# Kernel tuning notes

Hardware: AMD Instinct MI355X
Metric: run time of the kernel (lower is better)

The kernel has to match this reference:

```python
import jax, jax.numpy as jnp
import numpy as np


def _maxpool2(x):
    # x: [B, C, H, W] -> 2x2 max pool, stride 2
    b, c, h, w = x.shape
    return x.reshape(b, c, h // 2, 2, w // 2, 2).max(axis=(3, 5))


def _conv1x1(x, w, b):
    # x: [B, Cin, H, W], w: [Cout, Cin], b: [Cout]
    return jnp.einsum('bchw,oc->bohw', x, w) + b[None, :, None, None]


def setup_inputs() -> dict:
    key = jax.random.key(0)
    ks = jax.random.split(key, 8)
    C = 64
    B, H, W = 2, 128, 128
    s = 1.0 / np.sqrt(C)
    return {
        'x': jax.random.normal(ks[0], (B, C, H, W), jnp.float32),
        'w_theta': jax.random.normal(ks[1], (C // 8, C), jnp.float32) * s,
        'b_theta': jax.random.normal(ks[2], (C // 8,), jnp.float32) * s,
        'w_phi': jax.random.normal(ks[3], (C // 8, C), jnp.float32) * s,
        'b_phi': jax.random.normal(ks[4], (C // 8,), jnp.float32) * s,
        'w_g': jax.random.normal(ks[5], (C, C), jnp.float32) * s,
        'b_g': jax.random.normal(ks[6], (C,), jnp.float32) * s,
        'sigma_ratio': jnp.zeros((1,), jnp.float32) + 0.5,
    }


def reference(x, w_theta, b_theta, w_phi, b_phi, w_g, b_g, sigma_ratio):
    b, c, h, w = x.shape
    n = h * w
    # queries: [B, N, C//8]
    theta = _conv1x1(x, w_theta, b_theta).reshape(b, c // 8, n).transpose(0, 2, 1)
    # pooled keys: [B, C//8, N//4]
    phi = _maxpool2(_conv1x1(x, w_phi, b_phi)).reshape(b, c // 8, n // 4)
    # attention: [B, N, N//4] (unscaled, as in original)
    attn = jax.nn.softmax(jnp.einsum('bnd,bdm->bnm', theta, phi), axis=-1)
    # pooled values: [B, N//4, C]
    g = _maxpool2(_conv1x1(x, w_g, b_g)).reshape(b, c, n // 4).transpose(0, 2, 1)
    attn_g = jnp.einsum('bnm,bmc->bnc', attn, g)  # [B, N, C]
    attn_g = attn_g.transpose(0, 2, 1).reshape(b, c, h, w)
    return x + sigma_ratio * attn_g
```

## Files before the change

### kernel.cpp

```cpp
#include <hip/hip_runtime.h>
#include <hip/hip_bf16.h>

typedef _Float16 half8 __attribute__((ext_vector_type(8)));
typedef _Float16 f16x8 __attribute__((ext_vector_type(8)));
typedef __fp16 fp16x2 __attribute__((ext_vector_type(2)));
typedef __bf16 bf16x2v __attribute__((ext_vector_type(2)));
typedef __bf16 bf16x8 __attribute__((ext_vector_type(8)));
typedef float f32x16 __attribute__((ext_vector_type(16)));
typedef unsigned uint2v __attribute__((ext_vector_type(2)));

#define NPIX 16384
#define NPOOL 4096
#define BN 32768
#define KSPLIT 4
#define CHUNK 1024
#define NSTEP 8
#define LOG2E 1.44269504088896340736f

__device__ inline f32x16 mfma16(half8 a, half8 b, f32x16 c) {
  return __builtin_amdgcn_mfma_f32_32x32x16_f16(a, b, c, 0, 0, 0);
}
__device__ inline f32x16 mfma16b(bf16x8 a, bf16x8 b, f32x16 c) {
  return __builtin_amdgcn_mfma_f32_32x32x16_bf16(a, b, c, 0, 0, 0);
}
__device__ inline float fast_exp2(float x) {
#if __has_builtin(__builtin_amdgcn_exp2f)
  return __builtin_amdgcn_exp2f(x);
#else
  return exp2f(x);
#endif
}

__global__ __launch_bounds__(256) void prep_kernel(
    const float* __restrict__ x,
    const float* __restrict__ w_theta, const float* __restrict__ b_theta,
    const float* __restrict__ w_phi, const float* __restrict__ b_phi,
    const float* __restrict__ w_g, const float* __restrict__ b_g,
    _Float16* __restrict__ qf, _Float16* __restrict__ phiT,
    __bf16* __restrict__ gT) {
  __shared__ float xs[64][256];
  int bid = blockIdx.x;
  int oh = bid & 1;
  int pr = (bid >> 1) & 63;
  int b  = bid >> 7;
  int t = threadIdx.x;

  const float* xb = x + (size_t)b * 64 * NPIX + pr * 256;
#pragma unroll 8
  for (int c = 0; c < 64; c++) xs[c][t] = xb[(size_t)c * NPIX + t];
  __syncthreads();

  if (oh == 0) {
    float acc[8];
#pragma unroll
    for (int j = 0; j < 8; j++) acc[j] = b_theta[j];
#pragma unroll 4
    for (int c = 0; c < 64; c++) {
      float xv = xs[c][t];
#pragma unroll
      for (int j = 0; j < 8; j++) acc[j] += xv * w_theta[j * 64 + c];
    }
    half8 h;
#pragma unroll
    for (int j = 0; j < 8; j++) h[j] = (_Float16)(acc[j] * LOG2E);
    *(half8*)(qf + ((size_t)b * NPIX + pr * 256 + t) * 8) = h;
  }

  int pos = t & 63;
  int ocg = t >> 6;
  int oc0 = oh * 36 + ocg * 9;
  const float* wrow[9];
  float a0[9], a1[9], a2[9], a3[9];
#pragma unroll
  for (int j = 0; j < 9; j++) {
    int oc = oc0 + j;
    float bv;
    if (oc < 64) { wrow[j] = w_g + oc * 64; bv = b_g[oc]; }
    else         { wrow[j] = w_phi + (oc - 64) * 64; bv = b_phi[oc - 64]; }
    a0[j] = bv; a1[j] = bv; a2[j] = bv; a3[j] = bv;
  }
#pragma unroll 4
  for (int c = 0; c < 64; c++) {
    float2 lo = *(const float2*)&xs[c][2 * pos];
    float2 hi = *(const float2*)&xs[c][128 + 2 * pos];
#pragma unroll
    for (int j = 0; j < 9; j++) {
      float wv = wrow[j][c];
      a0[j] += wv * lo.x;
      a1[j] += wv * lo.y;
      a2[j] += wv * hi.x;
      a3[j] += wv * hi.y;
    }
  }
  int m = pr * 64 + pos;
#pragma unroll
  for (int j = 0; j < 9; j++) {
    int oc = oc0 + j;
    float v = fmaxf(fmaxf(a0[j], a1[j]), fmaxf(a2[j], a3[j]));
    if (oc < 64) gT[((size_t)b * 64 + oc) * NPOOL + m] = (__bf16)v;
    else         phiT[((size_t)b * NPOOL + m) * 8 + (oc - 64)] = (_Float16)v;
  }
}

__global__ __launch_bounds__(256, 4) void attn_kernel(
    const _Float16* __restrict__ qf, const _Float16* __restrict__ phiT,
    const __bf16* __restrict__ gT,
    float* __restrict__ part_l, _Float16* __restrict__ part_o) {
  __shared__ __bf16 lds_g[2][128 * 64];
  int bx = blockIdx.x;
  int kc = bx & (KSPLIT - 1);
  int qt = (bx >> 2) & 127;
  int b  = bx >> 9;
  int tid = threadIdx.x;
  int lane = tid & 63;
  int w = tid >> 6;
  int q = lane & 31, hi = lane >> 5;
  int qg0 = qt * 128 + w * 32;
  size_t qrow = (size_t)b * NPIX + qg0 + q;

  half8 qfrag = {0, 0, 0, 0, 0, 0, 0, 0};
  if (!hi) qfrag = *(const half8*)(qf + qrow * 8);

  f32x16 oacc0, oacc1;
#pragma unroll
  for (int i = 0; i < 16; i++) { oacc0[i] = 0.f; oacc1[i] = 0.f; }
  float lsum = 0.f;

  int kb0 = kc * CHUNK;

  const __bf16* gbase0;
  const __bf16* gbase1;
  {
    int c0 = (w * 2 + 0) * 8 + (lane >> 3);
    int c1 = (w * 2 + 1) * 8 + (lane >> 3);
    int s  = (lane & 7) ^ (lane >> 3);
    gbase0 = gT + ((size_t)b * 64 + c0) * NPOOL + 8 * s;
    gbase1 = gT + ((size_t)b * 64 + c1) * NPOOL + 8 * s;
  }
#define STAGE(buf, kb)                                                        \
  do {                                                                        \
    __builtin_amdgcn_global_load_lds(                                         \
        (const __attribute__((address_space(1))) void*)(gbase0 + (kb)),       \
        (__attribute__((address_space(3))) void*)((char*)&lds_g[buf][0] +     \
                                                  (w * 2 + 0) * 1024),        \
        16, 0, 0);                                                            \
    __builtin_amdgcn_global_load_lds(                                         \
        (const __attribute__((address_space(1))) void*)(gbase1 + (kb)),       \
        (__attribute__((address_space(3))) void*)((char*)&lds_g[buf][0] +     \
                                                  (w * 2 + 1) * 1024),        \
        16, 0, 0);                                                            \
    __builtin_amdgcn_global_load_lds(                                         \
        (const __attribute__((address_space(1))) void*)(gbase0 + (kb) + 64),  \
        (__attribute__((address_space(3))) void*)((char*)&lds_g[buf][0] +     \
                                                  8192 + (w * 2 + 0) * 1024), \
        16, 0, 0);                                                            \
    __builtin_amdgcn_global_load_lds(                                         \
        (const __attribute__((address_space(1))) void*)(gbase1 + (kb) + 64),  \
        (__attribute__((address_space(3))) void*)((char*)&lds_g[buf][0] +     \
                                                  8192 + (w * 2 + 1) * 1024), \
        16, 0, 0);                                                            \
  } while (0)

  STAGE(0, kb0);
  __syncthreads();
  int cur = 0;

#pragma unroll 1
  for (int step = 0; step < NSTEP; ++step) {
    int kb = kb0 + step * 128;
    if (step + 1 < NSTEP) STAGE(cur ^ 1, kb + 128);
#pragma unroll
    for (int kk = 0; kk < 2; ++kk) {
      int kbb = kb + kk * 64;
      half8 aphi0 = {0, 0, 0, 0, 0, 0, 0, 0}, aphi1 = aphi0;
      if (!hi) {
        aphi0 = *(const half8*)(phiT + ((size_t)b * NPOOL + kbb + q) * 8);
        aphi1 = *(const half8*)(phiT + ((size_t)b * NPOOL + kbb + 32 + q) * 8);
      }
      const __bf16* ldsb = &lds_g[cur][kk * 4096];
#pragma unroll
      for (int sub = 0; sub < 2; ++sub) {
        half8 aphi = sub ? aphi1 : aphi0;
        f32x16 sacc;
#pragma unroll
        for (int i = 0; i < 16; i++) sacc[i] = 0.f;
        sacc = mfma16(aphi, qfrag, sacc);
        float p[16];
#pragma unroll
        for (int i = 0; i < 16; i++) p[i] = fast_exp2(sacc[i]);
        lsum += (((p[0] + p[1]) + (p[2] + p[3])) + ((p[4] + p[5]) + (p[6] + p[7]))) +
                (((p[8] + p[9]) + (p[10] + p[11])) + ((p[12] + p[13]) + (p[14] + p[15])));
#pragma unroll
        for (int halfk = 0; halfk < 2; ++halfk) {
          int pb = halfk * 8;
          bf16x2v t0 = {(__bf16)p[pb + 0], (__bf16)p[pb + 1]};
          bf16x2v t1 = {(__bf16)p[pb + 2], (__bf16)p[pb + 3]};
          bf16x2v t2 = {(__bf16)p[pb + 4], (__bf16)p[pb + 5]};
          bf16x2v t3 = {(__bf16)p[pb + 6], (__bf16)p[pb + 7]};
          unsigned A0 = __builtin_bit_cast(unsigned, t0);
          unsigned A1 = __builtin_bit_cast(unsigned, t1);
          unsigned B0 = __builtin_bit_cast(unsigned, t2);
          unsigned B1 = __builtin_bit_cast(unsigned, t3);
          union { unsigned u[4]; bf16x8 h; } pf;
#if __has_builtin(__builtin_amdgcn_permlane32_swap)
          uint2v r0 = __builtin_amdgcn_permlane32_swap(A0, B0, false, false);
          uint2v r1 = __builtin_amdgcn_permlane32_swap(A1, B1, false, false);
          pf.u[0] = r0[0]; pf.u[1] = r1[0]; pf.u[2] = r0[1]; pf.u[3] = r1[1];
#else
          unsigned xA0 = __shfl_xor(A0, 32), xA1 = __shfl_xor(A1, 32);
          unsigned xB0 = __shfl_xor(B0, 32), xB1 = __shfl_xor(B1, 32);
          pf.u[0] = hi ? xB0 : A0;
          pf.u[1] = hi ? xB1 : A1;
          pf.u[2] = hi ? B0 : xA0;
          pf.u[3] = hi ? B1 : xA1;
#endif
          int sread = sub * 4 + halfk * 2 + hi;
          __builtin_amdgcn_s_setprio(1);
#pragma unroll
          for (int ct = 0; ct < 2; ++ct) {
            int row = ct * 32 + q;
            bf16x8 ag = *(const bf16x8*)(ldsb + row * 64 +
                                         (((16 * sread) ^ ((row & 7) << 4)) >> 1));
            if (ct == 0) oacc0 = mfma16b(ag, pf.h, oacc0);
            else         oacc1 = mfma16b(ag, pf.h, oacc1);
          }
          __builtin_amdgcn_s_setprio(0);
        }
      }
    }
    if (step + 1 < NSTEP) { __syncthreads(); cur ^= 1; }
  }
  lsum += __shfl_xor(lsum, 32);
  float rl = 1.0f / lsum;
  if (!hi) part_l[(size_t)kc * BN + qrow] = lsum;
  _Float16* po = part_o + (((size_t)(kc * 2 + b) * NPIX) + qg0 + q) * 64;
#pragma unroll
  for (int ct = 0; ct < 2; ++ct) {
#pragma unroll
    for (int g = 0; g < 4; ++g) {
      float v0 = (ct ? oacc1[4 * g + 0] : oacc0[4 * g + 0]) * rl;
      float v1 = (ct ? oacc1[4 * g + 1] : oacc0[4 * g + 1]) * rl;
      float v2 = (ct ? oacc1[4 * g + 2] : oacc0[4 * g + 2]) * rl;
      float v3 = (ct ? oacc1[4 * g + 3] : oacc0[4 * g + 3]) * rl;
      uint2v u;
      u[0] = __builtin_bit_cast(unsigned, __builtin_amdgcn_cvt_pkrtz(v0, v1));
      u[1] = __builtin_bit_cast(unsigned, __builtin_amdgcn_cvt_pkrtz(v2, v3));
      *(uint2v*)(po + 32 * ct + 8 * g + 4 * hi) = u;
    }
  }
}

__global__ __launch_bounds__(256) void reduce_kernel(
    const float* __restrict__ part_l, const _Float16* __restrict__ part_o,
    const float* __restrict__ x, const float* __restrict__ sig,
    float* __restrict__ out) {
  int t = threadIdx.x;
  int cg = t >> 6;
  int qi = blockIdx.x * 64 + (t & 63);
  int b = qi >> 14, n = qi & (NPIX - 1);
  float lv[KSPLIT], L = 0.f;
#pragma unroll
  for (int kc = 0; kc < KSPLIT; kc++) {
    lv[kc] = part_l[(size_t)kc * BN + qi];
    L += lv[kc];
  }
  float o16[16];
#pragma unroll
  for (int j = 0; j < 16; j++) o16[j] = 0.f;
#pragma unroll
  for (int kc = 0; kc < KSPLIT; kc++) {
    const _Float16* po = part_o + (((size_t)(kc * 2 + b) * NPIX) + n) * 64 + cg * 16;
    f16x8 v0 = *(const f16x8*)po;
    f16x8 v1 = *(const f16x8*)(po + 8);
    float wv = lv[kc];
#pragma unroll
    for (int j = 0; j < 8; j++) {
      o16[j]     += wv * (float)v0[j];
      o16[8 + j] += wv * (float)v1[j];
    }
  }
  float scale = sig[0] / L;
#pragma unroll
  for (int j = 0; j < 16; j++) {
    int c = cg * 16 + j;
    size_t idx = ((size_t)b * 64 + c) * NPIX + n;
    out[idx] = x[idx] + scale * o16[j];
  }
}

extern "C" void kernel_launch(void* const* d_in, const int* in_sizes, int n_in,
                              void* d_out, int out_size, void* d_ws, size_t ws_size,
                              hipStream_t stream) {
  const float* x       = (const float*)d_in[0];
  const float* w_theta = (const float*)d_in[1];
  const float* b_theta = (const float*)d_in[2];
  const float* w_phi   = (const float*)d_in[3];
  const float* b_phi   = (const float*)d_in[4];
  const float* w_g     = (const float*)d_in[5];
  const float* b_g     = (const float*)d_in[6];
  const float* sigma   = (const float*)d_in[7];
  float* out = (float*)d_out;

  char* ws = (char*)d_ws;
  _Float16* qf     = (_Float16*)ws;
  _Float16* phiT   = (_Float16*)(ws + 524288);
  __bf16*   gT     = (__bf16*)(ws + 655360);
  float*    part_l = (float*)(ws + 1703936);
  _Float16* part_o = (_Float16*)(ws + 2228224);

  prep_kernel<<<256, 256, 0, stream>>>(x, w_theta, b_theta, w_phi, b_phi,
                                       w_g, b_g, qf, phiT, gT);
  attn_kernel<<<2 * 128 * KSPLIT, 256, 0, stream>>>(qf, phiT, gT,
                                                    part_l, part_o);
  reduce_kernel<<<512, 256, 0, stream>>>(part_l, part_o, x, sigma, out);
}
```

Before: 63.80 us.

## Process two query tiles per wave and double the key split

Each wave now handles 64 queries as two 32-row fragments that share every LDS load of the pooled values and phi fragment. This halves LDS traffic per MFMA and gives more independent MFMA chains to interleave. The key dimension is split eight ways instead of four so the grid keeps the same block count. In exchange, accumulator registers roughly double (occupancy bound lowered to 3 blocks), and the larger partial-output buffer adds traffic to the reduce kernel.

```diff
diff --git a/kernel.cpp b/kernel.cpp
--- a/kernel.cpp
+++ b/kernel.cpp
@@ -3,7 +3,6 @@
 
 typedef _Float16 half8 __attribute__((ext_vector_type(8)));
 typedef _Float16 f16x8 __attribute__((ext_vector_type(8)));
-typedef __fp16 fp16x2 __attribute__((ext_vector_type(2)));
 typedef __bf16 bf16x2v __attribute__((ext_vector_type(2)));
 typedef __bf16 bf16x8 __attribute__((ext_vector_type(8)));
 typedef float f32x16 __attribute__((ext_vector_type(16)));
@@ -12,9 +11,9 @@
 #define NPIX 16384
 #define NPOOL 4096
 #define BN 32768
-#define KSPLIT 4
-#define CHUNK 1024
-#define NSTEP 8
+#define KSPLIT 8
+#define CHUNK 512
+#define NSTEP 4
 #define LOG2E 1.44269504088896340736f
 
 __device__ inline f32x16 mfma16(half8 a, half8 b, f32x16 c) {
@@ -102,29 +101,35 @@
   }
 }
 
-__global__ __launch_bounds__(256, 4) void attn_kernel(
+__global__ __launch_bounds__(256, 3) void attn_kernel(
     const _Float16* __restrict__ qf, const _Float16* __restrict__ phiT,
     const __bf16* __restrict__ gT,
     float* __restrict__ part_l, _Float16* __restrict__ part_o) {
   __shared__ __bf16 lds_g[2][128 * 64];
   int bx = blockIdx.x;
   int kc = bx & (KSPLIT - 1);
-  int qt = (bx >> 2) & 127;
+  int qt = (bx >> 3) & 63;
   int b  = bx >> 9;
   int tid = threadIdx.x;
   int lane = tid & 63;
   int w = tid >> 6;
   int q = lane & 31, hi = lane >> 5;
-  int qg0 = qt * 128 + w * 32;
-  size_t qrow = (size_t)b * NPIX + qg0 + q;
-
-  half8 qfrag = {0, 0, 0, 0, 0, 0, 0, 0};
-  if (!hi) qfrag = *(const half8*)(qf + qrow * 8);
-
-  f32x16 oacc0, oacc1;
-#pragma unroll
-  for (int i = 0; i < 16; i++) { oacc0[i] = 0.f; oacc1[i] = 0.f; }
-  float lsum = 0.f;
+  int qg0 = qt * 256 + w * 64;
+  size_t qrowA = (size_t)b * NPIX + qg0 + q;
+  size_t qrowB = qrowA + 32;
+
+  half8 qfragA = {0, 0, 0, 0, 0, 0, 0, 0}, qfragB = qfragA;
+  if (!hi) {
+    qfragA = *(const half8*)(qf + qrowA * 8);
+    qfragB = *(const half8*)(qf + qrowB * 8);
+  }
+
+  f32x16 oaccA0, oaccA1, oaccB0, oaccB1;
+#pragma unroll
+  for (int i = 0; i < 16; i++) {
+    oaccA0[i] = 0.f; oaccA1[i] = 0.f; oaccB0[i] = 0.f; oaccB1[i] = 0.f;
+  }
+  float lsumA = 0.f, lsumB = 0.f;
 
   int kb0 = kc * CHUNK;
 
@@ -181,38 +186,71 @@
 #pragma unroll
       for (int sub = 0; sub < 2; ++sub) {
         half8 aphi = sub ? aphi1 : aphi0;
-        f32x16 sacc;
-#pragma unroll
-        for (int i = 0; i < 16; i++) sacc[i] = 0.f;
-        sacc = mfma16(aphi, qfrag, sacc);
-        float p[16];
-#pragma unroll
-        for (int i = 0; i < 16; i++) p[i] = fast_exp2(sacc[i]);
-        lsum += (((p[0] + p[1]) + (p[2] + p[3])) + ((p[4] + p[5]) + (p[6] + p[7]))) +
-                (((p[8] + p[9]) + (p[10] + p[11])) + ((p[12] + p[13]) + (p[14] + p[15])));
+        f32x16 s0, s1;
+#pragma unroll
+        for (int i = 0; i < 16; i++) { s0[i] = 0.f; s1[i] = 0.f; }
+        s0 = mfma16(aphi, qfragA, s0);
+        s1 = mfma16(aphi, qfragB, s1);
+        unsigned uA[8], uB[8];
+        {
+          float p[16];
+#pragma unroll
+          for (int i = 0; i < 16; i++) p[i] = fast_exp2(s0[i]);
+          lsumA += (((p[0] + p[1]) + (p[2] + p[3])) + ((p[4] + p[5]) + (p[6] + p[7]))) +
+                   (((p[8] + p[9]) + (p[10] + p[11])) + ((p[12] + p[13]) + (p[14] + p[15])));
+#pragma unroll
+          for (int h = 0; h < 2; ++h) {
+            bf16x2v t0 = {(__bf16)p[h * 8 + 0], (__bf16)p[h * 8 + 1]};
+            bf16x2v t1 = {(__bf16)p[h * 8 + 2], (__bf16)p[h * 8 + 3]};
+            bf16x2v t2 = {(__bf16)p[h * 8 + 4], (__bf16)p[h * 8 + 5]};
+            bf16x2v t3 = {(__bf16)p[h * 8 + 6], (__bf16)p[h * 8 + 7]};
+            uA[h * 4 + 0] = __builtin_bit_cast(unsigned, t0);
+            uA[h * 4 + 1] = __builtin_bit_cast(unsigned, t1);
+            uA[h * 4 + 2] = __builtin_bit_cast(unsigned, t2);
+            uA[h * 4 + 3] = __builtin_bit_cast(unsigned, t3);
+          }
+        }
+        {
+          float p[16];
+#pragma unroll
+          for (int i = 0; i < 16; i++) p[i] = fast_exp2(s1[i]);
+          lsumB += (((p[0] + p[1]) + (p[2] + p[3])) + ((p[4] + p[5]) + (p[6] + p[7]))) +
+                   (((p[8] + p[9]) + (p[10] + p[11])) + ((p[12] + p[13]) + (p[14] + p[15])));
+#pragma unroll
+          for (int h = 0; h < 2; ++h) {
+            bf16x2v t0 = {(__bf16)p[h * 8 + 0], (__bf16)p[h * 8 + 1]};
+            bf16x2v t1 = {(__bf16)p[h * 8 + 2], (__bf16)p[h * 8 + 3]};
+            bf16x2v t2 = {(__bf16)p[h * 8 + 4], (__bf16)p[h * 8 + 5]};
+            bf16x2v t3 = {(__bf16)p[h * 8 + 6], (__bf16)p[h * 8 + 7]};
+            uB[h * 4 + 0] = __builtin_bit_cast(unsigned, t0);
+            uB[h * 4 + 1] = __builtin_bit_cast(unsigned, t1);
+            uB[h * 4 + 2] = __builtin_bit_cast(unsigned, t2);
+            uB[h * 4 + 3] = __builtin_bit_cast(unsigned, t3);
+          }
+        }
 #pragma unroll
         for (int halfk = 0; halfk < 2; ++halfk) {
-          int pb = halfk * 8;
-          bf16x2v t0 = {(__bf16)p[pb + 0], (__bf16)p[pb + 1]};
-          bf16x2v t1 = {(__bf16)p[pb + 2], (__bf16)p[pb + 3]};
-          bf16x2v t2 = {(__bf16)p[pb + 4], (__bf16)p[pb + 5]};
-          bf16x2v t3 = {(__bf16)p[pb + 6], (__bf16)p[pb + 7]};
-          unsigned A0 = __builtin_bit_cast(unsigned, t0);
-          unsigned A1 = __builtin_bit_cast(unsigned, t1);
-          unsigned B0 = __builtin_bit_cast(unsigned, t2);
-          unsigned B1 = __builtin_bit_cast(unsigned, t3);
-          union { unsigned u[4]; bf16x8 h; } pf;
+          union { unsigned u[4]; bf16x8 h; } pfA, pfB;
 #if __has_builtin(__builtin_amdgcn_permlane32_swap)
-          uint2v r0 = __builtin_amdgcn_permlane32_swap(A0, B0, false, false);
-          uint2v r1 = __builtin_amdgcn_permlane32_swap(A1, B1, false, false);
-          pf.u[0] = r0[0]; pf.u[1] = r1[0]; pf.u[2] = r0[1]; pf.u[3] = r1[1];
+          uint2v rA0 = __builtin_amdgcn_permlane32_swap(uA[halfk * 4 + 0], uA[halfk * 4 + 2], false, false);
+          uint2v rA1 = __builtin_amdgcn_permlane32_swap(uA[halfk * 4 + 1], uA[halfk * 4 + 3], false, false);
+          pfA.u[0] = rA0[0]; pfA.u[1] = rA1[0]; pfA.u[2] = rA0[1]; pfA.u[3] = rA1[1];
+          uint2v rB0 = __builtin_amdgcn_permlane32_swap(uB[halfk * 4 + 0], uB[halfk * 4 + 2], false, false);
+          uint2v rB1 = __builtin_amdgcn_permlane32_swap(uB[halfk * 4 + 1], uB[halfk * 4 + 3], false, false);
+          pfB.u[0] = rB0[0]; pfB.u[1] = rB1[0]; pfB.u[2] = rB0[1]; pfB.u[3] = rB1[1];
 #else
-          unsigned xA0 = __shfl_xor(A0, 32), xA1 = __shfl_xor(A1, 32);
-          unsigned xB0 = __shfl_xor(B0, 32), xB1 = __shfl_xor(B1, 32);
-          pf.u[0] = hi ? xB0 : A0;
-          pf.u[1] = hi ? xB1 : A1;
-          pf.u[2] = hi ? B0 : xA0;
-          pf.u[3] = hi ? B1 : xA1;
+          unsigned xA0 = __shfl_xor(uA[halfk * 4 + 0], 32), xA1 = __shfl_xor(uA[halfk * 4 + 1], 32);
+          unsigned xA2 = __shfl_xor(uA[halfk * 4 + 2], 32), xA3 = __shfl_xor(uA[halfk * 4 + 3], 32);
+          pfA.u[0] = hi ? xA2 : uA[halfk * 4 + 0];
+          pfA.u[1] = hi ? xA3 : uA[halfk * 4 + 1];
+          pfA.u[2] = hi ? uA[halfk * 4 + 2] : xA0;
+          pfA.u[3] = hi ? uA[halfk * 4 + 3] : xA1;
+          unsigned xB0 = __shfl_xor(uB[halfk * 4 + 0], 32), xB1 = __shfl_xor(uB[halfk * 4 + 1], 32);
+          unsigned xB2 = __shfl_xor(uB[halfk * 4 + 2], 32), xB3 = __shfl_xor(uB[halfk * 4 + 3], 32);
+          pfB.u[0] = hi ? xB2 : uB[halfk * 4 + 0];
+          pfB.u[1] = hi ? xB3 : uB[halfk * 4 + 1];
+          pfB.u[2] = hi ? uB[halfk * 4 + 2] : xB0;
+          pfB.u[3] = hi ? uB[halfk * 4 + 3] : xB1;
 #endif
           int sread = sub * 4 + halfk * 2 + hi;
           __builtin_amdgcn_s_setprio(1);
@@ -221,8 +259,8 @@
             int row = ct * 32 + q;
             bf16x8 ag = *(const bf16x8*)(ldsb + row * 64 +
                                          (((16 * sread) ^ ((row & 7) << 4)) >> 1));
-            if (ct == 0) oacc0 = mfma16b(ag, pf.h, oacc0);
-            else         oacc1 = mfma16b(ag, pf.h, oacc1);
+            if (ct == 0) { oaccA0 = mfma16b(ag, pfA.h, oaccA0); oaccB0 = mfma16b(ag, pfB.h, oaccB0); }
+            else         { oaccA1 = mfma16b(ag, pfA.h, oaccA1); oaccB1 = mfma16b(ag, pfB.h, oaccB1); }
           }
           __builtin_amdgcn_s_setprio(0);
         }
@@ -230,22 +268,35 @@
     }
     if (step + 1 < NSTEP) { __syncthreads(); cur ^= 1; }
   }
-  lsum += __shfl_xor(lsum, 32);
-  float rl = 1.0f / lsum;
-  if (!hi) part_l[(size_t)kc * BN + qrow] = lsum;
-  _Float16* po = part_o + (((size_t)(kc * 2 + b) * NPIX) + qg0 + q) * 64;
+  lsumA += __shfl_xor(lsumA, 32);
+  lsumB += __shfl_xor(lsumB, 32);
+  float rlA = 1.0f / lsumA, rlB = 1.0f / lsumB;
+  if (!hi) {
+    part_l[(size_t)kc * BN + qrowA] = lsumA;
+    part_l[(size_t)kc * BN + qrowB] = lsumB;
+  }
+  _Float16* poA = part_o + (((size_t)(kc * 2 + b) * NPIX) + qg0 + q) * 64;
+  _Float16* poB = poA + (size_t)32 * 64;
 #pragma unroll
   for (int ct = 0; ct < 2; ++ct) {
 #pragma unroll
-    for (int g = 0; g < 4; ++g) {
-      float v0 = (ct ? oacc1[4 * g + 0] : oacc0[4 * g + 0]) * rl;
-      float v1 = (ct ? oacc1[4 * g + 1] : oacc0[4 * g + 1]) * rl;
-      float v2 = (ct ? oacc1[4 * g + 2] : oacc0[4 * g + 2]) * rl;
-      float v3 = (ct ? oacc1[4 * g + 3] : oacc0[4 * g + 3]) * rl;
+    for (int cg = 0; cg < 4; ++cg) {
+      float a0 = (ct ? oaccA1[4 * cg + 0] : oaccA0[4 * cg + 0]) * rlA;
+      float a1 = (ct ? oaccA1[4 * cg + 1] : oaccA0[4 * cg + 1]) * rlA;
+      float a2 = (ct ? oaccA1[4 * cg + 2] : oaccA0[4 * cg + 2]) * rlA;
+      float a3 = (ct ? oaccA1[4 * cg + 3] : oaccA0[4 * cg + 3]) * rlA;
       uint2v u;
-      u[0] = __builtin_bit_cast(unsigned, __builtin_amdgcn_cvt_pkrtz(v0, v1));
-      u[1] = __builtin_bit_cast(unsigned, __builtin_amdgcn_cvt_pkrtz(v2, v3));
-      *(uint2v*)(po + 32 * ct + 8 * g + 4 * hi) = u;
+      u[0] = __builtin_bit_cast(unsigned, __builtin_amdgcn_cvt_pkrtz(a0, a1));
+      u[1] = __builtin_bit_cast(unsigned, __builtin_amdgcn_cvt_pkrtz(a2, a3));
+      *(uint2v*)(poA + 32 * ct + 8 * cg + 4 * hi) = u;
+      float b0 = (ct ? oaccB1[4 * cg + 0] : oaccB0[4 * cg + 0]) * rlB;
+      float b1 = (ct ? oaccB1[4 * cg + 1] : oaccB0[4 * cg + 1]) * rlB;
+      float b2 = (ct ? oaccB1[4 * cg + 2] : oaccB0[4 * cg + 2]) * rlB;
+      float b3 = (ct ? oaccB1[4 * cg + 3] : oaccB0[4 * cg + 3]) * rlB;
+      uint2v v;
+      v[0] = __builtin_bit_cast(unsigned, __builtin_amdgcn_cvt_pkrtz(b0, b1));
+      v[1] = __builtin_bit_cast(unsigned, __builtin_amdgcn_cvt_pkrtz(b2, b3));
+      *(uint2v*)(poB + 32 * ct + 8 * cg + 4 * hi) = v;
     }
   }
 }
@@ -306,11 +357,11 @@
   _Float16* phiT   = (_Float16*)(ws + 524288);
   __bf16*   gT     = (__bf16*)(ws + 655360);
   float*    part_l = (float*)(ws + 1703936);
-  _Float16* part_o = (_Float16*)(ws + 2228224);
+  _Float16* part_o = (_Float16*)(ws + 2752512);
 
   prep_kernel<<<256, 256, 0, stream>>>(x, w_theta, b_theta, w_phi, b_phi,
                                        w_g, b_g, qf, phiT, gT);
-  attn_kernel<<<2 * 128 * KSPLIT, 256, 0, stream>>>(qf, phiT, gT,
-                                                    part_l, part_o);
+  attn_kernel<<<2 * 64 * KSPLIT, 256, 0, stream>>>(qf, phiT, gT,
+                                                   part_l, part_o);
   reduce_kernel<<<512, 256, 0, stream>>>(part_l, part_o, x, sigma, out);
 }
```

Result: slower. 144.4 us (+126.3%).
